# Kernel tuning notes

Measured on AMD Instinct MI355X. Metric: run time of the kernel, lower is better.

The kernel has to match this reference:

```python
import jax, jax.numpy as jnp
import numpy as np

NMS_THRESH = 0.7   # cfg.NMS_THRESHOLD
POST_NMS = 1000    # cfg.POST_NMS_TEST (training=False)


def get_roi(anchors, offset):
    # R-CNN box decode, center format {x, y, w, h}
    sx, sy, sw, sh = jnp.split(anchors, 4, axis=-1)
    ox, oy, ow, oh = jnp.split(offset, 4, axis=-1)
    return jnp.concatenate([sw * ox + sx,
                            sh * oy + sy,
                            sw * jnp.exp(ow),
                            sh * jnp.exp(oh)], axis=-1)


def center2corner(boxes):
    x, y, w, h = jnp.split(boxes, 4, axis=-1)
    return jnp.concatenate([x - w / 2, y - h / 2, x + w / 2, y + h / 2], axis=-1)


def nms_keep(boxes, thresh):
    # boxes: [N,4] corner format, already sorted by score descending
    N = boxes.shape[0]
    x1, y1, x2, y2 = boxes[:, 0], boxes[:, 1], boxes[:, 2], boxes[:, 3]
    areas = (x2 - x1) * (y2 - y1)
    idx = jnp.arange(N)

    def body(i, keep):
        xx1 = jnp.maximum(x1[i], x1)
        yy1 = jnp.maximum(y1[i], y1)
        xx2 = jnp.minimum(x2[i], x2)
        yy2 = jnp.minimum(y2[i], y2)
        inter = jnp.maximum(xx2 - xx1, 0.0) * jnp.maximum(yy2 - yy1, 0.0)
        iou = inter / (areas[i] + areas - inter + 1e-9)
        sup = (iou > thresh) & (idx > i) & keep[i]
        return keep & (~sup)

    return jax.lax.fori_loop(0, N, body, jnp.ones(N, dtype=bool))


def setup_inputs() -> dict:
    key = jax.random.key(0)
    k1, k2, k3, k4, k5 = jax.random.split(key, 5)
    B, N = 8, 16384
    H, W = 600, 800
    cx = jax.random.uniform(k1, (B, N, 1)) * W
    cy = jax.random.uniform(k2, (B, N, 1)) * H
    wh = 16.0 + jax.random.uniform(k3, (B, N, 2)) * 240.0
    anchors = jnp.concatenate([cx, cy, wh], axis=-1)          # [B,N,4] center fmt
    reg_scores = jax.random.normal(k4, (B, N, 4)) * 0.1        # box offsets
    fg_scores = jax.random.normal(k5, (B, N))                  # objectness
    return {"fg_scores": fg_scores, "reg_scores": reg_scores,
            "anchors": anchors, "img_h": H, "img_w": W}


def reference(fg_scores, reg_scores, anchors, img_h, img_w):
    # decode -> corners -> clip to image
    rois = get_roi(anchors, reg_scores)                        # [B,N,4]
    corners = center2corner(rois)
    x = jnp.clip(corners[..., 0::2], 0.0, img_w - 1)           # x1, x2
    y = jnp.clip(corners[..., 1::2], 0.0, img_h - 1)           # y1, y2
    boxes = jnp.stack([x[..., 0], y[..., 0], x[..., 1], y[..., 1]], axis=-1)

    # sort per image by score descending
    order = jnp.argsort(-fg_scores, axis=-1)                   # [B,N]
    boxes_sorted = jnp.take_along_axis(boxes, order[..., None], axis=1)

    # per-image greedy NMS (index decisions are non-differentiable constants)
    keep = jax.lax.stop_gradient(
        jax.vmap(lambda b: nms_keep(b, NMS_THRESH))(boxes_sorted))  # [B,N] bool

    # first POST_NMS kept indices, in score order (stable sort: kept first)
    kept_idx = jnp.argsort(~keep, axis=-1, stable=True)[:, :POST_NMS]  # [B,P]
    valid = jnp.arange(POST_NMS)[None, :] < keep.sum(axis=-1, keepdims=True)
    boxes_out = jnp.take_along_axis(boxes_sorted, kept_idx[..., None], axis=1)
    boxes_out = boxes_out * valid[..., None]                   # zero-pad tail
    kept_idx = jnp.where(valid, kept_idx, -1)
    return boxes_out, kept_idx, valid
```

## Files before the change

kernel.cpp:

```cpp
#include <hip/hip_runtime.h>
#include <stdint.h>
#include <math.h>

#define BATCH 8
#define NPB   16384
#define HALF  8192
#define POST  1000
#define ACC_CAP 2046

#define KSEL 3584
#define SCAP 4096
#define NBKT 8192

typedef unsigned long long u64;

#define W1F 799.0f
#define H1F 599.0f

#define IOU_B (0.699999988079071044921875 + 0x1.0p-25)

__device__ __forceinline__ bool iou_gt(float x1, float y1, float x2, float y2, float area,
                                       float kx1, float ky1, float kx2, float ky2, float kar) {
  float xx1 = fmaxf(x1, kx1);
  float yy1 = fmaxf(y1, ky1);
  float xx2 = fminf(x2, kx2);
  float yy2 = fminf(y2, ky2);
  float iw = fmaxf(__fsub_rn(xx2, xx1), 0.0f);
  float ih = fmaxf(__fsub_rn(yy2, yy1), 0.0f);
  float inter = __fmul_rn(iw, ih);
  float mx = fmaxf(kar, area);
  if (!(inter >= __fmul_rn(0.69f, mx))) return false;
  float den = __fadd_rn(__fsub_rn(__fadd_rn(kar, area), inter), 1e-9f);
  return __fdiv_rn(inter, den) > 0.7f;
}

__device__ __forceinline__ void decode_one(const float4* a4, const float4* r4, int orig,
                                           float& x1, float& y1, float& x2, float& y2) {
  float4 a = a4[orig];
  float4 r = r4[orig];
  float cx = __fadd_rn(__fmul_rn(a.z, r.x), a.x);
  float cy = __fadd_rn(__fmul_rn(a.w, r.y), a.y);
  float w  = __fmul_rn(a.z, expf(r.z));
  float h  = __fmul_rn(a.w, expf(r.w));
  float hw = __fmul_rn(w, 0.5f);
  float hh = __fmul_rn(h, 0.5f);
  x1 = fminf(fmaxf(__fsub_rn(cx, hw), 0.0f), W1F);
  y1 = fminf(fmaxf(__fsub_rn(cy, hh), 0.0f), H1F);
  x2 = fminf(fmaxf(__fadd_rn(cx, hw), 0.0f), W1F);
  y2 = fminf(fmaxf(__fadd_rn(cy, hh), 0.0f), H1F);
}

__device__ __forceinline__ float area_of(float x1, float y1, float x2, float y2) {
  return __fmul_rn(__fsub_rn(x2, x1), __fsub_rn(y2, y1));
}

__device__ __forceinline__ u64 shfl_xor_u64(u64 v, int m) {
  unsigned lo = __shfl_xor((unsigned)v, m, 64);
  unsigned hi = __shfl_xor((unsigned)(v >> 32), m, 64);
  return ((u64)hi << 32) | lo;
}

__global__ __launch_bounds__(1024) void select_sort_decode_kernel(
    const float* __restrict__ fg, const float* __restrict__ anc,
    const float* __restrict__ reg, float4* __restrict__ sbox,
    float* __restrict__ sarea, int* __restrict__ selC1) {
  __shared__ char smem[65536];
  unsigned* hist = (unsigned*)smem;
  u64* sb = (u64*)(smem + 32768);
  unsigned* scratch = (unsigned*)(smem + 32768);

  int b = blockIdx.x;
  int tid = threadIdx.x;
  int lane = tid & 63;
  int wave = tid >> 6;
  const float* fgb = fg + (size_t)b * NPB;

  for (int i = tid; i < NBKT; i += 1024) hist[i] = 0u;
  __syncthreads();

  unsigned mkey[16];
  #pragma unroll
  for (int k = 0; k < 16; ++k) {
    unsigned u = __float_as_uint(fgb[tid + k * 1024]);
    unsigned t = u ^ 0x80000000u;
    mkey[k] = (t & 0x80000000u) ? ~t : (t | 0x80000000u);
  }
  #pragma unroll
  for (int k = 0; k < 16; ++k) atomicAdd(&hist[mkey[k] >> 19], 1u);
  __syncthreads();

  unsigned p0 = 0;
  #pragma unroll
  for (int j = 0; j < 8; ++j) p0 += hist[tid * 8 + j];
  unsigned pI = p0;
  #pragma unroll
  for (int d = 1; d < 64; d <<= 1) {
    unsigned o = __shfl_up(pI, d, 64);
    if (lane >= d) pI += o;
  }
  if (lane == 63) scratch[1024 + wave] = pI;
  __syncthreads();
  if (wave == 0) {
    unsigned s = (lane < 16) ? scratch[1024 + lane] : 0u;
    #pragma unroll
    for (int d = 1; d < 16; d <<= 1) {
      unsigned o = __shfl_up(s, d, 64);
      if (lane >= d) s += o;
    }
    if (lane < 16) scratch[1040 + lane] = s;
  }
  __syncthreads();
  unsigned base = (wave == 0) ? 0u : scratch[1040 + wave - 1];
  unsigned myIncl = base + pI;
  unsigned myExcl = myIncl - p0;
  if (myExcl < (unsigned)KSEL && myIncl >= (unsigned)KSEL) {
    unsigned cum = myExcl;
    for (int j = 0; j < 8; ++j) {
      cum += hist[tid * 8 + j];
      if (cum >= (unsigned)KSEL) {
        scratch[1056] = (unsigned)(tid * 8 + j);
        scratch[1057] = cum;
        break;
      }
    }
  }
  __syncthreads();
  unsigned b0 = scratch[1056];
  int c1 = (int)scratch[1057];
  __syncthreads();

  if (tid == 0) {
    selC1[b] = c1;
    hist[0] = 0u;
  }
  for (int i = tid; i < SCAP; i += 1024) sb[i] = ~0ull;
  __syncthreads();
  if (c1 > SCAP) return;

  u64 lowmask = (1ull << lane) - 1ull;
  #pragma unroll
  for (int k = 0; k < 16; ++k) {
    bool sel = ((mkey[k] >> 19) <= b0);
    u64 act = __ballot(sel);
    if (act) {
      int leader = __builtin_ctzll(act);
      unsigned wbase = 0;
      if (lane == leader) wbase = atomicAdd(&hist[0], (unsigned)__popcll(act));
      wbase = __shfl(wbase, leader, 64);
      if (sel) {
        unsigned pos = wbase + (unsigned)__popcll(act & lowmask);
        sb[pos] = ((u64)mkey[k] << 32) | (unsigned)(tid + k * 1024);
      }
    }
  }
  __syncthreads();

  int c1chunks = (c1 + 63) >> 6;
  for (int c = wave; c < SCAP / 64; c += 16) {
    if (c >= c1chunks) continue;
    int i = c * 64 + lane;
    u64 v = sb[i];
    #pragma unroll
    for (int k = 2; k <= 64; k <<= 1) {
      #pragma unroll
      for (int j = k >> 1; j > 0; j >>= 1) {
        u64 o = shfl_xor_u64(v, j);
        bool up = ((i & k) == 0);
        bool keepMin = (((lane & j) == 0) == up);
        bool less = (v < o);
        v = (keepMin == less) ? v : o;
      }
    }
    sb[i] = v;
  }
  __syncthreads();
  for (int k = 128; k <= SCAP; k <<= 1) {
    for (int j = k >> 1; j >= 64; j >>= 1) {
      for (int tt = tid; tt < SCAP / 2; tt += 1024) {
        int i = ((tt & ~(j - 1)) << 1) | (tt & (j - 1));
        int p = i | j;
        bool up = ((i & k) == 0);
        u64 va = sb[i], vc = sb[p];
        if ((va > vc) == up) { sb[i] = vc; sb[p] = va; }
      }
      __syncthreads();
    }
    for (int c = wave; c < SCAP / 64; c += 16) {
      int i = c * 64 + lane;
      u64 v = sb[i];
      bool up = ((i & k) == 0);
      #pragma unroll
      for (int j = 32; j > 0; j >>= 1) {
        u64 o = shfl_xor_u64(v, j);
        bool keepMin = (((lane & j) == 0) == up);
        bool less = (v < o);
        v = (keepMin == less) ? v : o;
      }
      sb[i] = v;
    }
    __syncthreads();
  }

  const float4* a4 = (const float4*)anc + (size_t)b * NPB;
  const float4* r4 = (const float4*)reg + (size_t)b * NPB;
  for (int rank = tid; rank < c1; rank += 1024) {
    u64 v = sb[rank];
    int orig = (int)(v & 0xFFFFu);
    float x1, y1, x2, y2;
    decode_one(a4, r4, orig, x1, y1, x2, y2);
    size_t idx = (size_t)b * NPB + rank;
    sbox[idx]  = make_float4(x1, y1, x2, y2);
    sarea[idx] = area_of(x1, y1, x2, y2);
  }
}

__global__ __launch_bounds__(256) void iou_matrix_kernel(const float4* __restrict__ sbox,
                                                         const float* __restrict__ sarea,
                                                         u64* __restrict__ mat,
                                                         int T, int tilesPB) {
  __shared__ float4 sRB[256];
  __shared__ float  sRA[256];
  int wg = blockIdx.x;
  int b  = wg / tilesPB;
  int t  = wg % tilesPB;
  int rb = (int)((sqrtf(8.0f * (float)t + 1.0f) - 1.0f) * 0.5f);
  while ((rb + 1) * (rb + 2) / 2 <= t) ++rb;
  while (rb * (rb + 1) / 2 > t) --rb;
  int sbk = t - rb * (rb + 1) / 2;

  const float4* bb = sbox + (size_t)b * NPB;
  const float*  ba = sarea + (size_t)b * NPB;
  int tid = threadIdx.x;

  sRB[tid] = bb[rb * 256 + tid];
  sRA[tid] = ba[rb * 256 + tid];
  __syncthreads();

  int wave = tid >> 6, lane = tid & 63;
  u64* matb = mat + (size_t)b * ((size_t)(T >> 6) * (size_t)T);

  int s = sbk * 256 + wave * 64 + lane;
  float4 sbx = bb[s];
  float  sar = ba[s];
  u64* dst = matb + (size_t)(sbk * 4 + wave) * (size_t)T + (size_t)(rb * 256);
  const double Bq = IOU_B;

  int rg0 = (rb == sbk) ? wave : 0;
  for (int rg = rg0; rg < 4; ++rg) {
    u64 my = 0ull;
    #pragma unroll
    for (int u = 0; u < 64; ++u) {
      int rl = rg * 64 + u;
      float4 rbx = sRB[rl];
      float  rar = sRA[rl];
      float xx1 = fmaxf(rbx.x, sbx.x);
      float yy1 = fmaxf(rbx.y, sbx.y);
      float xx2 = fminf(rbx.z, sbx.z);
      float yy2 = fminf(rbx.w, sbx.w);
      float iw = fmaxf(__fsub_rn(xx2, xx1), 0.0f);
      float ih = fmaxf(__fsub_rn(yy2, yy1), 0.0f);
      float inter = __fmul_rn(iw, ih);
      float den = __fadd_rn(__fsub_rn(__fadd_rn(rar, sar), inter), 1e-9f);
      u64 wd = __ballot((double)inter >= Bq * (double)den);
      if (lane == u) my = wd;
    }
    dst[rg * 64 + lane] = my;
  }
}

__global__ __launch_bounds__(1024) void nms_reduce_kernel(const float4* __restrict__ sbox,
                                                          const float* __restrict__ sarea,
                                                          const u64* __restrict__ mat,
                                                          float* __restrict__ out, int T,
                                                          const int* __restrict__ selC1,
                                                          const float* __restrict__ fg,
                                                          const float* __restrict__ reg,
                                                          const float* __restrict__ anc,
                                                          u64* __restrict__ keys) {
  __shared__ alignas(16) char smem[65536];
  float4* acc = (float4*)smem;
  u64* kmask = (u64*)(smem + 32768);
  int* s_cnt = (int*)(smem + 34816);

  int b = blockIdx.x;
  int tid = threadIdx.x;
  int lane = tid & 63;
  int wave = tid >> 6;
  int C1 = selC1[b];
  if (C1 > SCAP) C1 = 0;

  const float4* bb = sbox + (size_t)b * NPB;
  const float*  ba = sarea + (size_t)b * NPB;
  const u64* matb = mat + (size_t)b * ((size_t)(T >> 6) * (size_t)T);

  if (tid == 0) *s_cnt = 0;
  __syncthreads();

  if (wave == 0 && T > 0 && C1 > 0) {
    int cnt = 0;
    int Wmax = T >> 6;
    u64 lowmask = (1ull << lane) - 1ull;
    for (int w = 0; w < Wmax; ++w) {
      if (cnt >= POST) break;
      int r = (w << 6) + lane;
      u64 orr = 0ull;
      for (int v = 0; v < w; ++v)
        orr |= matb[(size_t)v * T + r] & kmask[v];
      bool sup = (orr != 0ull);
      u64 own = matb[(size_t)w * T + r] & lowmask;

      u64 avail = __ballot(!sup);
      u64 deps = own & avail;
      u64 km = 0ull, fin = 0ull;
      while ((avail & ~fin) != 0ull) {
        bool mine   = ((avail & ~fin) >> lane) & 1ull;
        bool ready  = mine && ((deps & ~fin) == 0ull);
        bool keepme = ready && ((own & km) == 0ull);
        u64 rdy = __ballot(ready);
        u64 kp  = __ballot(keepme);
        fin |= rdy;
        km  |= kp;
      }

      if (lane == 0) kmask[w] = km;
      if ((km >> lane) & 1ull) {
        int d = cnt + __popcll(km & lowmask);
        float4 mb = bb[r];
        acc[d] = mb;
        if (d < POST) {
          size_t bo = (size_t)b * POST * 4 + (size_t)d * 4;
          out[bo + 0] = mb.x;
          out[bo + 1] = mb.y;
          out[bo + 2] = mb.z;
          out[bo + 3] = mb.w;
          out[(size_t)BATCH * POST * 4 + (size_t)b * POST + d] = (float)r;
          out[(size_t)BATCH * POST * 5 + (size_t)b * POST + d] = 1.0f;
        }
      }
      cnt += __popcll(km);
    }
    if (lane == 0) *s_cnt = cnt;
  }
  __syncthreads();

  for (int base = T; base < C1; base += 1024) {
    int cnt0 = *s_cnt;
    if (cnt0 >= POST) break;
    int pos = base + tid;
    bool inr = (pos < C1);
    float4 mybox = bb[inr ? pos : 0];
    float area = ba[inr ? pos : 0];
    float x1 = mybox.x, y1 = mybox.y, x2 = mybox.z, y2 = mybox.w;
    bool sup = !inr;

    for (int ai = 0; ai < cnt0; ++ai) {
      float4 ab = acc[ai];
      float aar = area_of(ab.x, ab.y, ab.z, ab.w);
      if (!sup && iou_gt(x1, y1, x2, y2, area, ab.x, ab.y, ab.z, ab.w, aar)) sup = true;
    }

    for (int w = 0; w < 16; ++w) {
      int cbase = *s_cnt;
      __syncthreads();
      if (wave == w) {
        u64 undec = __ballot(!sup);
        u64 km = 0ull;
        while (undec) {
          int l = __builtin_ctzll(undec);
          km |= (1ull << l);
          float kx1 = __shfl(x1, l);
          float ky1 = __shfl(y1, l);
          float kx2 = __shfl(x2, l);
          float ky2 = __shfl(y2, l);
          float kar = __shfl(area, l);
          if (lane > l && !sup) {
            if (iou_gt(x1, y1, x2, y2, area, kx1, ky1, kx2, ky2, kar)) sup = true;
          }
          undec = __ballot(!sup) & ~((2ull << l) - 1ull);
        }
        int nnew = __popcll(km);
        if ((km >> lane) & 1ull) {
          int d = cbase + __popcll(km & ((1ull << lane) - 1ull));
          acc[d] = make_float4(x1, y1, x2, y2);
          if (d < POST) {
            size_t bo = (size_t)b * POST * 4 + (size_t)d * 4;
            out[bo + 0] = x1;
            out[bo + 1] = y1;
            out[bo + 2] = x2;
            out[bo + 3] = y2;
            out[(size_t)BATCH * POST * 4 + (size_t)b * POST + d] = (float)pos;
            out[(size_t)BATCH * POST * 5 + (size_t)b * POST + d] = 1.0f;
          }
        }
        if (lane == 0) *s_cnt = cbase + nnew;
      }
      __syncthreads();
      int cnew = *s_cnt;
      if (wave > w && !sup) {
        for (int ai = cbase; ai < cnew; ++ai) {
          float4 ab = acc[ai];
          float aar = area_of(ab.x, ab.y, ab.z, ab.w);
          if (iou_gt(x1, y1, x2, y2, area, ab.x, ab.y, ab.z, ab.w, aar)) {
            sup = true; break;
          }
        }
      }
      __syncthreads();
    }
  }
  __syncthreads();

  int total = *s_cnt;

  if (total >= POST) {
    return;
  }

  {
    u64* sb = (u64*)smem;
    unsigned short* ord = (unsigned short*)smem;
    float4* racc = (float4*)(smem + 32768);
    int* r_cnt = (int*)(smem + 65504);

    u64* kb = keys + (size_t)b * NPB;
    const float* fgb = fg + (size_t)b * NPB;
    __syncthreads();

    for (int h = 1; h >= 0; --h) {
      for (int i = tid; i < HALF; i += 1024) {
        int g = h * HALF + i;
        unsigned u = __float_as_uint(fgb[g]);
        unsigned t = u ^ 0x80000000u;
        unsigned m = (t & 0x80000000u) ? ~t : (t | 0x80000000u);
        sb[i] = ((u64)m << 32) | (unsigned)g;
      }
      __syncthreads();
      for (int k = 2; k <= HALF; k <<= 1) {
        for (int j = k >> 1; j > 0; j >>= 1) {
          for (int tt = tid; tt < HALF / 2; tt += 1024) {
            int i = ((tt & ~(j - 1)) << 1) | (tt & (j - 1));
            int p = i | j;
            bool up = (((i & k) == 0) == (h == 0));
            u64 va = sb[i], vc = sb[p];
            if ((va > vc) == up) { sb[i] = vc; sb[p] = va; }
          }
          __syncthreads();
        }
      }
      if (h == 1) {
        for (int i = tid; i < HALF; i += 1024) kb[HALF + i] = sb[i];
        __syncthreads();
      }
    }

    for (int i = tid; i < HALF; i += 1024) {
      u64 a = sb[i], c = kb[HALF + i];
      if (a > c) { sb[i] = c; kb[HALF + i] = a; }
    }
    __syncthreads();

    for (int j = HALF >> 1; j > 0; j >>= 1) {
      for (int tt = tid; tt < HALF / 2; tt += 1024) {
        int i = ((tt & ~(j - 1)) << 1) | (tt & (j - 1));
        int p = i | j;
        u64 va = sb[i], vc = sb[p];
        if (va > vc) { sb[i] = vc; sb[p] = va; }
      }
      __syncthreads();
    }
    for (int i = tid; i < HALF; i += 1024) kb[i] = sb[i];
    __syncthreads();

    for (int i = tid; i < HALF; i += 1024) sb[i] = kb[HALF + i];
    __syncthreads();
    for (int j = HALF >> 1; j > 0; j >>= 1) {
      for (int tt = tid; tt < HALF / 2; tt += 1024) {
        int i = ((tt & ~(j - 1)) << 1) | (tt & (j - 1));
        int p = i | j;
        u64 va = sb[i], vc = sb[p];
        if (va > vc) { sb[i] = vc; sb[p] = va; }
      }
      __syncthreads();
    }
    for (int i = tid; i < HALF; i += 1024) kb[HALF + i] = sb[i];
    __syncthreads();

    for (int i = tid; i < NPB; i += 1024) ord[i] = (unsigned short)(kb[i] & 0xFFFFu);
    if (tid == 0) *r_cnt = 0;
    __syncthreads();

    const float4* a4 = (const float4*)anc + (size_t)b * NPB;
    const float4* r4 = (const float4*)reg + (size_t)b * NPB;

    for (int base2 = 0; base2 < NPB; base2 += 1024) {
      int cnt0 = *r_cnt;
      if (cnt0 >= POST) break;
      int pos = base2 + tid;
      int orig = ord[pos];
      float x1, y1, x2, y2;
      decode_one(a4, r4, orig, x1, y1, x2, y2);
      float area = area_of(x1, y1, x2, y2);

      bool sup = false;
      for (int ai = 0; ai < cnt0; ++ai) {
        float4 ab = racc[ai];
        float aar = area_of(ab.x, ab.y, ab.z, ab.w);
        if (!sup && iou_gt(x1, y1, x2, y2, area, ab.x, ab.y, ab.z, ab.w, aar)) sup = true;
      }

      for (int w = 0; w < 16; ++w) {
        int cbase = *r_cnt;
        __syncthreads();
        if (wave == w) {
          u64 undec = __ballot(!sup);
          u64 km = 0ull;
          while (undec) {
            int l = __builtin_ctzll(undec);
            km |= (1ull << l);
            float kx1 = __shfl(x1, l);
            float ky1 = __shfl(y1, l);
            float kx2 = __shfl(x2, l);
            float ky2 = __shfl(y2, l);
            float kar = __shfl(area, l);
            if (lane > l && !sup) {
              if (iou_gt(x1, y1, x2, y2, area, kx1, ky1, kx2, ky2, kar)) sup = true;
            }
            undec = __ballot(!sup) & ~((2ull << l) - 1ull);
          }
          int nnew = __popcll(km);
          if ((km >> lane) & 1ull) {
            int d = cbase + __popcll(km & ((1ull << lane) - 1ull));
            racc[d] = make_float4(x1, y1, x2, y2);
            if (d < POST) {
              size_t bo = (size_t)b * POST * 4 + (size_t)d * 4;
              out[bo + 0] = x1;
              out[bo + 1] = y1;
              out[bo + 2] = x2;
              out[bo + 3] = y2;
              out[(size_t)BATCH * POST * 4 + (size_t)b * POST + d] = (float)pos;
              out[(size_t)BATCH * POST * 5 + (size_t)b * POST + d] = 1.0f;
            }
          }
          if (lane == 0) *r_cnt = cbase + nnew;
        }
        __syncthreads();
        int cnew = *r_cnt;
        if (wave > w && !sup) {
          for (int ai = cbase; ai < cnew; ++ai) {
            float4 ab = racc[ai];
            float aar = area_of(ab.x, ab.y, ab.z, ab.w);
            if (iou_gt(x1, y1, x2, y2, area, ab.x, ab.y, ab.z, ab.w, aar)) {
              sup = true; break;
            }
          }
        }
        __syncthreads();
      }
    }
    __syncthreads();

    total = *r_cnt;
  }

  for (int s = tid; s < POST; s += 1024) {
    if (s >= total) {
      size_t bo = (size_t)b * POST * 4 + (size_t)s * 4;
      out[bo + 0] = 0.0f;
      out[bo + 1] = 0.0f;
      out[bo + 2] = 0.0f;
      out[bo + 3] = 0.0f;
      out[(size_t)BATCH * POST * 4 + (size_t)b * POST + s] = -1.0f;
      out[(size_t)BATCH * POST * 5 + (size_t)b * POST + s] = 0.0f;
    }
  }
}

extern "C" void kernel_launch(void* const* d_in, const int* in_sizes, int n_in,
                              void* d_out, int out_size, void* d_ws, size_t ws_size,
                              hipStream_t stream) {
  (void)in_sizes; (void)n_in; (void)out_size;
  const float* fg  = (const float*)d_in[0];
  const float* reg = (const float*)d_in[1];
  const float* anc = (const float*)d_in[2];
  float* out = (float*)d_out;

  char* ws = (char*)d_ws;
  u64*    keys  = (u64*)ws;
  float4* sbox  = (float4*)(ws + ((size_t)1 << 20));
  float*  sarea = (float*)(ws + ((size_t)3 << 20));
  int*    selC1 = (int*)(ws + ((size_t)3 << 20) + 524288);
  u64*    mat   = (u64*)(ws + ((size_t)4 << 20));

  size_t avail = (ws_size > ((size_t)4 << 20)) ? (ws_size - ((size_t)4 << 20)) : 0;
  int T = 0;
  if      (avail >= (size_t)8 * 48 * 3072 * 8) T = 3072;
  else if (avail >= (size_t)8 * 32 * 2048 * 8) T = 2048;

  select_sort_decode_kernel<<<BATCH, 1024, 0, stream>>>(fg, anc, reg, sbox, sarea, selC1);
  if (T > 0) {
    int NTB = T >> 8;
    int tilesPB = NTB * (NTB + 1) / 2;
    iou_matrix_kernel<<<BATCH * tilesPB, 256, 0, stream>>>(sbox, sarea, mat, T, tilesPB);
  }
  nms_reduce_kernel<<<BATCH, 1024, 0, stream>>>(sbox, sarea, mat, out, T, selC1,
                                                fg, reg, anc, keys);
}
```

Baseline: 177.9 us.

## Replace bitonic sort with bucket scatter and in-bucket rank counting

```diff
diff --git a/kernel.cpp b/kernel.cpp
--- a/kernel.cpp
+++ b/kernel.cpp
@@ -54,12 +54,6 @@
   return __fmul_rn(__fsub_rn(x2, x1), __fsub_rn(y2, y1));
 }
 
-__device__ __forceinline__ u64 shfl_xor_u64(u64 v, int m) {
-  unsigned lo = __shfl_xor((unsigned)v, m, 64);
-  unsigned hi = __shfl_xor((unsigned)(v >> 32), m, 64);
-  return ((u64)hi << 32) | lo;
-}
-
 __global__ __launch_bounds__(1024) void select_sort_decode_kernel(
     const float* __restrict__ fg, const float* __restrict__ anc,
     const float* __restrict__ reg, float4* __restrict__ sbox,
@@ -111,106 +105,53 @@
   }
   __syncthreads();
   unsigned base = (wave == 0) ? 0u : scratch[1040 + wave - 1];
-  unsigned myIncl = base + pI;
-  unsigned myExcl = myIncl - p0;
-  if (myExcl < (unsigned)KSEL && myIncl >= (unsigned)KSEL) {
-    unsigned cum = myExcl;
-    for (int j = 0; j < 8; ++j) {
-      cum += hist[tid * 8 + j];
-      if (cum >= (unsigned)KSEL) {
-        scratch[1056] = (unsigned)(tid * 8 + j);
-        scratch[1057] = cum;
-        break;
-      }
-    }
+  unsigned running = base + pI - p0;
+  #pragma unroll
+  for (int j = 0; j < 8; ++j) {
+    unsigned c = hist[tid * 8 + j];
+    if (running < (unsigned)KSEL && running + c >= (unsigned)KSEL) {
+      scratch[1056] = (unsigned)(tid * 8 + j);
+      scratch[1057] = running + c;
+    }
+    hist[tid * 8 + j] = running;
+    running += c;
   }
   __syncthreads();
   unsigned b0 = scratch[1056];
   int c1 = (int)scratch[1057];
   __syncthreads();
 
-  if (tid == 0) {
-    selC1[b] = c1;
-    hist[0] = 0u;
-  }
-  for (int i = tid; i < SCAP; i += 1024) sb[i] = ~0ull;
-  __syncthreads();
+  if (tid == 0) selC1[b] = c1;
   if (c1 > SCAP) return;
 
-  u64 lowmask = (1ull << lane) - 1ull;
   #pragma unroll
   for (int k = 0; k < 16; ++k) {
-    bool sel = ((mkey[k] >> 19) <= b0);
-    u64 act = __ballot(sel);
-    if (act) {
-      int leader = __builtin_ctzll(act);
-      unsigned wbase = 0;
-      if (lane == leader) wbase = atomicAdd(&hist[0], (unsigned)__popcll(act));
-      wbase = __shfl(wbase, leader, 64);
-      if (sel) {
-        unsigned pos = wbase + (unsigned)__popcll(act & lowmask);
-        sb[pos] = ((u64)mkey[k] << 32) | (unsigned)(tid + k * 1024);
-      }
-    }
-  }
-  __syncthreads();
-
-  int c1chunks = (c1 + 63) >> 6;
-  for (int c = wave; c < SCAP / 64; c += 16) {
-    if (c >= c1chunks) continue;
-    int i = c * 64 + lane;
-    u64 v = sb[i];
-    #pragma unroll
-    for (int k = 2; k <= 64; k <<= 1) {
-      #pragma unroll
-      for (int j = k >> 1; j > 0; j >>= 1) {
-        u64 o = shfl_xor_u64(v, j);
-        bool up = ((i & k) == 0);
-        bool keepMin = (((lane & j) == 0) == up);
-        bool less = (v < o);
-        v = (keepMin == less) ? v : o;
-      }
-    }
-    sb[i] = v;
-  }
-  __syncthreads();
-  for (int k = 128; k <= SCAP; k <<= 1) {
-    for (int j = k >> 1; j >= 64; j >>= 1) {
-      for (int tt = tid; tt < SCAP / 2; tt += 1024) {
-        int i = ((tt & ~(j - 1)) << 1) | (tt & (j - 1));
-        int p = i | j;
-        bool up = ((i & k) == 0);
-        u64 va = sb[i], vc = sb[p];
-        if ((va > vc) == up) { sb[i] = vc; sb[p] = va; }
-      }
-      __syncthreads();
-    }
-    for (int c = wave; c < SCAP / 64; c += 16) {
-      int i = c * 64 + lane;
-      u64 v = sb[i];
-      bool up = ((i & k) == 0);
-      #pragma unroll
-      for (int j = 32; j > 0; j >>= 1) {
-        u64 o = shfl_xor_u64(v, j);
-        bool keepMin = (((lane & j) == 0) == up);
-        bool less = (v < o);
-        v = (keepMin == less) ? v : o;
-      }
-      sb[i] = v;
-    }
-    __syncthreads();
-  }
+    unsigned B = mkey[k] >> 19;
+    if (B <= b0) {
+      unsigned pos = atomicAdd(&hist[B], 1u);
+      sb[pos] = ((u64)mkey[k] << 32) | (unsigned)(tid + k * 1024);
+    }
+  }
+  __syncthreads();
 
   const float4* a4 = (const float4*)anc + (size_t)b * NPB;
   const float4* r4 = (const float4*)reg + (size_t)b * NPB;
-  for (int rank = tid; rank < c1; rank += 1024) {
-    u64 v = sb[rank];
-    int orig = (int)(v & 0xFFFFu);
-    float x1, y1, x2, y2;
-    decode_one(a4, r4, orig, x1, y1, x2, y2);
-    size_t idx = (size_t)b * NPB + rank;
-    sbox[idx]  = make_float4(x1, y1, x2, y2);
-    sarea[idx] = area_of(x1, y1, x2, y2);
+  #pragma unroll
+  for (int k = 0; k < 16; ++k) {
+    unsigned B = mkey[k] >> 19;
+    if (B <= b0) {
+      unsigned lo = (B != 0u) ? hist[B - 1] : 0u;
+      unsigned hi = hist[B];
+      u64 myk = ((u64)mkey[k] << 32) | (unsigned)(tid + k * 1024);
+      unsigned cnt = 0;
+      for (unsigned p = lo; p < hi; ++p) cnt += (sb[p] < myk) ? 1u : 0u;
+      int rank = (int)(lo + cnt);
+      float x1, y1, x2, y2;
+      decode_one(a4, r4, (int)(tid + k * 1024), x1, y1, x2, y2);
+      size_t idx = (size_t)b * NPB + rank;
+      sbox[idx]  = make_float4(x1, y1, x2, y2);
+      sarea[idx] = area_of(x1, y1, x2, y2);
+    }
   }
 }
 
```

Result: slower. 348.1 us (+95.6%).
